# Kernel tuning notes

Hardware: AMD Instinct MI355X
Metric: run time of the kernel (lower is better)

The kernel has to match this reference:

```python
import jax, jax.numpy as jnp
import numpy as np

KSIZE = 7
FEAT_SIZE = 64
BETA = 0.02


def _resize_bilinear_ac(x, out_h, out_w):
    """Bilinear resize with align_corners=True. x: (B, C, H, W)."""
    H, W = x.shape[-2], x.shape[-1]
    ys = jnp.linspace(0.0, H - 1.0, out_h)
    xs = jnp.linspace(0.0, W - 1.0, out_w)
    y0 = jnp.clip(jnp.floor(ys).astype(jnp.int32), 0, H - 1)
    x0 = jnp.clip(jnp.floor(xs).astype(jnp.int32), 0, W - 1)
    y1 = jnp.minimum(y0 + 1, H - 1)
    x1 = jnp.minimum(x0 + 1, W - 1)
    wy = (ys - y0.astype(x.dtype))[None, None, :, None]
    wx = (xs - x0.astype(x.dtype))[None, None, None, :]
    rows = x[:, :, y0, :] * (1.0 - wy) + x[:, :, y1, :] * wy      # (B,C,out_h,W)
    out = rows[:, :, :, x0] * (1.0 - wx) + rows[:, :, :, x1] * wx  # (B,C,out_h,out_w)
    return out


def _sce(feat, w, b):
    """EfficientSpatialContextNet: shifted local-correlation context + 1x1 conv + relu."""
    B, C, h, wd = feat.shape
    k, pad = KSIZE, KSIZE // 2
    # F.normalize(p=2, dim=1) with eps=1e-12 (clamped norm)
    fn = feat / jnp.maximum(jnp.sqrt(jnp.sum(feat * feat, axis=1, keepdims=True)), 1e-12)
    fp = jnp.pad(fn, ((0, 0), (0, 0), (pad, pad), (pad, pad)))
    offsets = ([(i, i) for i in range(k)]
               + [(i, pad) for i in range(k)]
               + [(i, k - 1 - i) for i in range(k)]
               + [(pad, i) for i in range(k)])
    ctx = jnp.stack([jnp.sum(fp[:, :, r:h + r, c:wd + c] * fn, axis=1)
                     for (r, c) in offsets], axis=1)  # (B, 4k, h, w)
    out = jnp.concatenate([feat, ctx], axis=1)        # (B, C+4k, h, w)
    out = jnp.einsum('oc,bchw->bohw', w, out) + b[None, :, None, None]
    return jax.nn.relu(out)


def _l2norm(f):
    # FeatureL2Norm: eps added inside sqrt
    return f / jnp.sqrt(jnp.sum(f * f, axis=1, keepdims=True) + 1e-6)


def _forward(src_feat, tgt_feat, sce_w, sce_b):
    fs = FEAT_SIZE
    s = _l2norm(_sce(src_feat, sce_w, sce_b))
    t = _l2norm(_sce(tgt_feat, sce_w, sce_b))
    B, C, hs, ws = s.shape
    ht, wt = t.shape[2], t.shape[3]
    Ls, Lt = hs * ws, ht * wt
    corr = jnp.einsum('bcs,bct->bst', s.reshape(B, C, Ls), t.reshape(B, C, Lt))
    # mutual NN filter (Rocco et al.)
    smax = jnp.max(corr, axis=2, keepdims=True)
    tmax = jnp.max(corr, axis=1, keepdims=True)
    smax = jnp.where(smax == 0, 1e-30, smax)
    tmax = jnp.where(tmax == 0, 1e-30, tmax)
    corr = corr * ((corr / smax) * (corr / tmax))
    # resize corr on source grid, then on target grid (bilinear, align_corners=True)
    c_s2t = jnp.transpose(corr, (0, 2, 1)).reshape(B, Lt, hs, ws)
    c_s2t = _resize_bilinear_ac(c_s2t, fs, fs)                       # (B, Lt, fs, fs)
    c_t2s = jnp.transpose(c_s2t.reshape(B, Lt, fs * fs), (0, 2, 1)).reshape(B, fs * fs, ht, wt)
    c = _resize_bilinear_ac(c_t2s, fs, fs)                           # (B, fs*fs, fs, fs)
    # soft argmax with temperature (softmax over source positions)
    p = jax.nn.softmax(c / BETA, axis=1).reshape(B, fs, fs, fs, fs)  # (B, hs', ws', ht', wt')
    xn = jnp.linspace(-1.0, 1.0, fs).astype(c.dtype)
    yn = jnp.linspace(-1.0, 1.0, fs).astype(c.dtype)
    grid_x = jnp.einsum('bijhw,j->bhw', p, xn)
    grid_y = jnp.einsum('bijhw,i->bhw', p, yn)
    flow_norm = jnp.stack([grid_x, grid_y], axis=1)                  # (B, 2, fs, fs)
    # unnormalise mapping and convert to flow
    H = W = fs
    mx = (flow_norm[:, 0] + 1.0) * (W - 1) / 2.0
    my = (flow_norm[:, 1] + 1.0) * (H - 1) / 2.0
    xx = jnp.arange(W, dtype=flow_norm.dtype)[None, None, :]
    yy = jnp.arange(H, dtype=flow_norm.dtype)[None, :, None]
    flow = jnp.stack([mx - xx, my - yy], axis=1)                     # (B, 2, fs, fs)
    return flow


def setup_inputs() -> dict:
    key = jax.random.key(0)
    k1, k2, k3 = jax.random.split(key, 3)
    B, C, h, w = 4, 1024, 32, 32
    src_feat = jax.random.normal(k1, (B, C, h, w), dtype=jnp.float32)
    tgt_feat = jax.random.normal(k2, (B, C, h, w), dtype=jnp.float32)
    sce_w = jax.random.normal(k3, (2048, C + 4 * KSIZE), dtype=jnp.float32) * 0.03
    sce_b = jnp.zeros((2048,), dtype=jnp.float32)
    return {"src_feat": src_feat, "tgt_feat": tgt_feat, "sce_w": sce_w, "sce_b": sce_b}


def reference(src_feat, tgt_feat, sce_w, sce_b):
    return _forward(src_feat, tgt_feat, sce_w, sce_b)
```

## Files before the change

### kernel.cpp

```cpp
#include <hip/hip_runtime.h>
#include <math.h>

#define HW    1024
#define CIN   1024
#define CCTX  28
#define CALL  1052
#define COUT  2048
#define CCHNK 512

typedef _Float16 half8   __attribute__((ext_vector_type(8)));
typedef _Float16 half4_t __attribute__((ext_vector_type(4)));
typedef _Float16 half2_t __attribute__((ext_vector_type(2)));
typedef __fp16   fp16x2  __attribute__((ext_vector_type(2)));
typedef float    f32x4   __attribute__((ext_vector_type(4)));

__device__ __forceinline__ void split2(float a0, float a1, half2_t& h, half2_t& l) {
    float h0 = __uint_as_float(__float_as_uint(a0) & 0xFFFFE000u);
    float h1 = __uint_as_float(__float_as_uint(a1) & 0xFFFFE000u);
    fp16x2 hp = __builtin_amdgcn_cvt_pkrtz(h0, h1);
    fp16x2 lp = __builtin_amdgcn_cvt_pkrtz(a0 - h0, a1 - h1);
    h = __builtin_bit_cast(half2_t, hp);
    l = __builtin_bit_cast(half2_t, lp);
}
__device__ __forceinline__ void split4(float4 v, half4_t& h, half4_t& l) {
    half2_t ha, la, hb, lb;
    split2(v.x, v.y, ha, la);
    split2(v.z, v.w, hb, lb);
    h = __builtin_shufflevector(ha, hb, 0, 1, 2, 3);
    l = __builtin_shufflevector(la, lb, 0, 1, 2, 3);
}
__device__ __forceinline__ float f4get(const float4& v, int e) {
    return e == 0 ? v.x : e == 1 ? v.y : e == 2 ? v.z : v.w;
}

__global__ void pnorm_part(const float* __restrict__ src, const float* __restrict__ tgt,
                           float* __restrict__ parts) {
    int img = blockIdx.x, pb = blockIdx.y, part = blockIdx.z;
    int p = pb * 64 + threadIdx.x;
    const float* feat = ((img < 4) ? src + (size_t)img * CIN * HW
                                   : tgt + (size_t)(img - 4) * CIN * HW)
                        + (size_t)part * 256 * HW + p;
    float a4[4] = {};
    for (int c = 0; c < 256; c += 8) {
        float v[8];
#pragma unroll
        for (int j = 0; j < 8; ++j) v[j] = feat[(size_t)(c + j) * HW];
#pragma unroll
        for (int j = 0; j < 8; ++j) a4[j & 3] = fmaf(v[j], v[j], a4[j & 3]);
    }
    parts[(size_t)part * 8192 + img * 1024 + p] = (a4[0] + a4[1]) + (a4[2] + a4[3]);
}
__global__ void pnorm_combine(const float* __restrict__ parts, float* __restrict__ pnorm) {
    int img = blockIdx.x;
    int p = blockIdx.y * 64 + threadIdx.x;
    float s = parts[img * 1024 + p] + parts[8192 + img * 1024 + p]
            + parts[16384 + img * 1024 + p] + parts[24576 + img * 1024 + p];
    pnorm[img * HW + p] = fmaxf(sqrtf(s), 1e-12f);
}

__global__ void ctx_kernel(const float* __restrict__ src, const float* __restrict__ tgt,
                           const float* __restrict__ pnorm, float* __restrict__ ctx) {
    int img = blockIdx.x;
    int y = blockIdx.y;
    int tid = threadIdx.x;
    int o = tid >> 5;
    int x = tid & 31;
    const float* feat = (img < 4) ? src + (size_t)img * CIN * HW
                                  : tgt + (size_t)(img - 4) * CIN * HW;
    int g = o / 7, i = o % 7;
    int r, c;
    if (g == 0)      { r = i; c = i; }
    else if (g == 1) { r = i; c = 3; }
    else if (g == 2) { r = i; c = 6 - i; }
    else             { r = 3; c = i; }
    int y2 = y + r - 3, x2 = x + c - 3;
    int p = y * 32 + x;
    float outv = 0.f;
    if (y2 >= 0 && y2 < 32 && x2 >= 0 && x2 < 32) {
        int p2 = y2 * 32 + x2;
        const float* f0 = feat + p;
        const float* f1 = feat + p2;
        float a4[4] = {};
        for (int ch = 0; ch < CIN; ch += 8) {
            float va[8], vb[8];
#pragma unroll
            for (int j = 0; j < 8; ++j) {
                va[j] = f0[(size_t)(ch + j) * HW];
                vb[j] = f1[(size_t)(ch + j) * HW];
            }
#pragma unroll
            for (int j = 0; j < 8; ++j) a4[j & 3] = fmaf(va[j], vb[j], a4[j & 3]);
        }
        float acc = (a4[0] + a4[1]) + (a4[2] + a4[3]);
        outv = acc / (pnorm[img * HW + p] * pnorm[img * HW + p2]);
    }
    ctx[((size_t)img * CCTX + o) * HW + p] = outv;
}

#define ABUF_H 2560
#define BBUF_H 5120
#define BUF_H  15360
template <bool FIRST>
__global__ __launch_bounds__(256, 2) void conv_mfma(
    const float* __restrict__ src, const float* __restrict__ tgt,
    const float* __restrict__ ctxb, const float* __restrict__ w,
    const float* __restrict__ bias, float* __restrict__ ychunk,
    float* __restrict__ nrm_parts, int c0) {
    __shared__ __align__(16) _Float16 lds[2 * BUF_H];

    int cb = blockIdx.x, pb = blockIdx.y, img = blockIdx.z;
    int n0 = pb * 64, m0g = c0 + cb * 128;
    const float* feat = (img < 4) ? src + (size_t)img * CIN * HW
                                  : tgt + (size_t)(img - 4) * CIN * HW;
    const float* ctxi = ctxb + (size_t)img * CCTX * HW;
    int tid = threadIdx.x;
    int aq = tid & 15, ar = tid >> 4;
    int brow = tid >> 1, bh_ = tid & 1;

    float4 xa[2], xb[4];
    auto loadA = [&](int k0) {
#pragma unroll
        for (int j = 0; j < 2; ++j) {
            int k = k0 + ar * 2 + j;
            if (k < CIN)       xa[j] = *(const float4*)(feat + (size_t)k * HW + n0 + aq * 4);
            else if (k < CALL) xa[j] = *(const float4*)(ctxi + (size_t)(k - CIN) * HW + n0 + aq * 4);
            else               xa[j] = make_float4(0.f, 0.f, 0.f, 0.f);
        }
    };
    auto loadB = [&](int k0) {
#pragma unroll
        for (int i = 0; i < 4; ++i) {
            int k = k0 + bh_ * 16 + i * 4;
            xb[i] = (k < CALL) ? *(const float4*)(w + (size_t)(m0g + brow) * CALL + k)
                               : make_float4(0.f, 0.f, 0.f, 0.f);
        }
    };
    auto storeLDS = [&](int b) {
        _Float16* Ah = lds + b * BUF_H;
        _Float16* Al = Ah + ABUF_H;
        _Float16* Bh = Al + ABUF_H;
        _Float16* Bl = Bh + BBUF_H;
#pragma unroll
        for (int p = 0; p < 4; ++p) {
            half2_t h, l;
            split2(f4get(xa[0], p), f4get(xa[1], p), h, l);
            int row = aq * 4 + p;
            *(half2_t*)(Ah + row * 40 + ar * 2) = h;
            *(half2_t*)(Al + row * 40 + ar * 2) = l;
        }
#pragma unroll
        for (int i = 0; i < 4; ++i) {
            half4_t h, l;
            split4(xb[i], h, l);
            *(half4_t*)(Bh + brow * 40 + bh_ * 16 + i * 4) = h;
            *(half4_t*)(Bl + brow * 40 + bh_ * 16 + i * 4) = l;
        }
    };

    int lane = tid & 63, wv4 = tid >> 6;
    int wm = wv4 >> 1, wn = wv4 & 1;
    int frow = lane & 15, kcol = (lane >> 4) * 8;

    f32x4 acc[2][4] = {};
    const int NT = 33;
    loadA(0); loadB(0); storeLDS(0);
    __syncthreads();
    for (int t = 0; t < NT; ++t) {
        if (t + 1 < NT) { loadA((t + 1) * 32); loadB((t + 1) * 32); }
        const _Float16* Ah = lds + (t & 1) * BUF_H;
        const _Float16* Al = Ah + ABUF_H;
        const _Float16* Bh = Al + ABUF_H;
        const _Float16* Bl = Bh + BBUF_H;
        half8 ah[2], alr[2], bhr[4], blr[4];
#pragma unroll
        for (int fm = 0; fm < 2; ++fm) {
            int r = wm * 32 + fm * 16 + frow;
            ah[fm]  = *(const half8*)(Ah + r * 40 + kcol);
            alr[fm] = *(const half8*)(Al + r * 40 + kcol);
        }
#pragma unroll
        for (int fn = 0; fn < 4; ++fn) {
            int r = wn * 64 + fn * 16 + frow;
            bhr[fn] = *(const half8*)(Bh + r * 40 + kcol);
            blr[fn] = *(const half8*)(Bl + r * 40 + kcol);
        }
#pragma unroll
        for (int fm = 0; fm < 2; ++fm)
#pragma unroll
            for (int fn = 0; fn < 4; ++fn) {
                acc[fm][fn] = __builtin_amdgcn_mfma_f32_16x16x32_f16(ah[fm],  bhr[fn], acc[fm][fn], 0, 0, 0);
                acc[fm][fn] = __builtin_amdgcn_mfma_f32_16x16x32_f16(ah[fm],  blr[fn], acc[fm][fn], 0, 0, 0);
                acc[fm][fn] = __builtin_amdgcn_mfma_f32_16x16x32_f16(alr[fm], bhr[fn], acc[fm][fn], 0, 0, 0);
            }
        if (t + 1 < NT) storeLDS((t + 1) & 1);
        __syncthreads();
    }

    float* ybounce = (float*)lds;
    float* ns = ybounce + 64 * 132;
    float psum[2][4] = {};
#pragma unroll
    for (int fm = 0; fm < 2; ++fm)
#pragma unroll
        for (int fn = 0; fn < 4; ++fn) {
            int chan_l = wn * 64 + fn * 16 + (lane & 15);
            float bv = bias[m0g + chan_l];
#pragma unroll
            for (int r = 0; r < 4; ++r) {
                float v = fmaxf(acc[fm][fn][r] + bv, 0.f);
                int pix_l = wm * 32 + fm * 16 + (lane >> 4) * 4 + r;
                ybounce[pix_l * 132 + chan_l] = v;
                psum[fm][r] = fmaf(v, v, psum[fm][r]);
            }
        }
#pragma unroll
    for (int off = 1; off <= 8; off <<= 1)
#pragma unroll
        for (int fm = 0; fm < 2; ++fm)
#pragma unroll
            for (int r = 0; r < 4; ++r)
                psum[fm][r] = psum[fm][r] + __shfl_xor(psum[fm][r], off);
    if ((lane & 15) == 0) {
#pragma unroll
        for (int fm = 0; fm < 2; ++fm)
#pragma unroll
            for (int r = 0; r < 4; ++r)
                ns[wn * 64 + wm * 32 + fm * 16 + (lane >> 4) * 4 + r] = psum[fm][r];
    }
    __syncthreads();
    {
        int row = tid >> 2, seg = tid & 3;
        float* yp = ychunk + ((size_t)img * HW + n0 + row) * CCHNK + cb * 128 + seg * 32;
#pragma unroll
        for (int i = 0; i < 8; ++i)
            *(float4*)(yp + i * 4) = *(float4*)(ybounce + row * 132 + seg * 32 + i * 4);
    }
    if (tid < 64) {
        float sv = ns[tid] + ns[64 + tid];
        float* np = nrm_parts + ((size_t)img * 4 + cb) * HW + n0 + tid;
        if (FIRST) *np = sv; else *np += sv;
    }
}

template <int MODE>
__global__ __launch_bounds__(256, 2) void corr_mfma(
    const float* __restrict__ ychunk, const float* __restrict__ nrm_sq,
    float* __restrict__ corrT, float* __restrict__ spar, float* __restrict__ tpar) {
    __shared__ __align__(16) _Float16 lds[2 * BUF_H];

    int sb = blockIdx.x, tb = blockIdx.y, b = blockIdx.z;
    int t0 = tb * 64, s0 = sb * 128;
    const float* ytg = ychunk + (size_t)(4 + b) * HW * CCHNK;
    const float* ysr = ychunk + (size_t)b * HW * CCHNK;
    int tid = threadIdx.x;
    int arow = tid >> 2, akq = tid & 3;
    int brow = tid >> 1, bh_ = tid & 1;

    float4 xa[2], xb[4];
    auto loadAB = [&](int k0) {
#pragma unroll
        for (int i = 0; i < 2; ++i)
            xa[i] = *(const float4*)(ytg + (size_t)(t0 + arow) * CCHNK + k0 + akq * 8 + i * 4);
#pragma unroll
        for (int i = 0; i < 4; ++i)
            xb[i] = *(const float4*)(ysr + (size_t)(s0 + brow) * CCHNK + k0 + bh_ * 16 + i * 4);
    };
    auto storeLDS = [&](int bb) {
        _Float16* Ah = lds + bb * BUF_H;
        _Float16* Al = Ah + ABUF_H;
        _Float16* Bh = Al + ABUF_H;
        _Float16* Bl = Bh + BBUF_H;
#pragma unroll
        for (int i = 0; i < 2; ++i) {
            half4_t h, l;
            split4(xa[i], h, l);
            *(half4_t*)(Ah + arow * 40 + akq * 8 + i * 4) = h;
            *(half4_t*)(Al + arow * 40 + akq * 8 + i * 4) = l;
        }
#pragma unroll
        for (int i = 0; i < 4; ++i) {
            half4_t h, l;
            split4(xb[i], h, l);
            *(half4_t*)(Bh + brow * 40 + bh_ * 16 + i * 4) = h;
            *(half4_t*)(Bl + brow * 40 + bh_ * 16 + i * 4) = l;
        }
    };

    int lane = tid & 63, wv4 = tid >> 6;
    int wm = wv4 >> 1, wn = wv4 & 1;
    int frow = lane & 15, kcol = (lane >> 4) * 8;

    f32x4 acc[2][4] = {};
    const int NT = CCHNK / 32;
    loadAB(0); storeLDS(0);
    __syncthreads();
    for (int t = 0; t < NT; ++t) {
        if (t + 1 < NT) loadAB((t + 1) * 32);
        const _Float16* Ah = lds + (t & 1) * BUF_H;
        const _Float16* Al = Ah + ABUF_H;
        const _Float16* Bh = Al + ABUF_H;
        const _Float16* Bl = Bh + BBUF_H;
        half8 ah[2], alr[2], bhr[4], blr[4];
#pragma unroll
        for (int fm = 0; fm < 2; ++fm) {
            int r = wm * 32 + fm * 16 + frow;
            ah[fm]  = *(const half8*)(Ah + r * 40 + kcol);
            alr[fm] = *(const half8*)(Al + r * 40 + kcol);
        }
#pragma unroll
        for (int fn = 0; fn < 4; ++fn) {
            int r = wn * 64 + fn * 16 + frow;
            bhr[fn] = *(const half8*)(Bh + r * 40 + kcol);
            blr[fn] = *(const half8*)(Bl + r * 40 + kcol);
        }
#pragma unroll
        for (int fm = 0; fm < 2; ++fm)
#pragma unroll
            for (int fn = 0; fn < 4; ++fn) {
                acc[fm][fn] = __builtin_amdgcn_mfma_f32_16x16x32_f16(ah[fm],  bhr[fn], acc[fm][fn], 0, 0, 0);
                acc[fm][fn] = __builtin_amdgcn_mfma_f32_16x16x32_f16(ah[fm],  blr[fn], acc[fm][fn], 0, 0, 0);
                acc[fm][fn] = __builtin_amdgcn_mfma_f32_16x16x32_f16(alr[fm], bhr[fn], acc[fm][fn], 0, 0, 0);
            }
        if (t + 1 < NT) storeLDS((t + 1) & 1);
        __syncthreads();
    }

    float rnt[2][4], rns[4];
    float rowmax[2][4] = {};
    float colmax[4] = {};
    if (MODE == 2) {
#pragma unroll
        for (int fm = 0; fm < 2; ++fm)
#pragma unroll
            for (int r = 0; r < 4; ++r) {
                int t = t0 + wm * 32 + fm * 16 + (lane >> 4) * 4 + r;
                rnt[fm][r] = 1.f / sqrtf(nrm_sq[(size_t)(4 + b) * HW + t] + 1e-6f);
            }
#pragma unroll
        for (int fn = 0; fn < 4; ++fn) {
            int s_ = s0 + wn * 64 + fn * 16 + (lane & 15);
            rns[fn] = 1.f / sqrtf(nrm_sq[(size_t)b * HW + s_] + 1e-6f);
        }
    }
#pragma unroll
    for (int fm = 0; fm < 2; ++fm)
#pragma unroll
        for (int r = 0; r < 4; ++r) {
            int t = t0 + wm * 32 + fm * 16 + (lane >> 4) * 4 + r;
            float* cp = corrT + ((size_t)b * HW + t) * HW + s0 + wn * 64 + (lane & 15);
#pragma unroll
            for (int fn = 0; fn < 4; ++fn) {
                float v = acc[fm][fn][r];
                if (MODE >= 1) v += cp[fn * 16];
                if (MODE == 2) {
                    v *= rnt[fm][r] * rns[fn];
                    rowmax[fm][r] = fmaxf(rowmax[fm][r], v);
                    colmax[fn] = fmaxf(colmax[fn], v);
                }
                cp[fn * 16] = v;
            }
        }
    if (MODE == 2) {
        float* rm = (float*)lds;
        float* cm = rm + 128;
#pragma unroll
        for (int off = 1; off <= 8; off <<= 1)
#pragma unroll
            for (int fm = 0; fm < 2; ++fm)
#pragma unroll
                for (int r = 0; r < 4; ++r)
                    rowmax[fm][r] = fmaxf(rowmax[fm][r], __shfl_xor(rowmax[fm][r], off));
        if ((lane & 15) == 0) {
#pragma unroll
            for (int fm = 0; fm < 2; ++fm)
#pragma unroll
                for (int r = 0; r < 4; ++r)
                    rm[wn * 64 + wm * 32 + fm * 16 + (lane >> 4) * 4 + r] = rowmax[fm][r];
        }
#pragma unroll
        for (int off = 16; off <= 32; off <<= 1)
#pragma unroll
            for (int fn = 0; fn < 4; ++fn)
                colmax[fn] = fmaxf(colmax[fn], __shfl_xor(colmax[fn], off));
        if ((lane >> 4) == 0) {
#pragma unroll
            for (int fn = 0; fn < 4; ++fn)
                cm[wv4 * 64 + fn * 16 + (lane & 15)] = colmax[fn];
        }
        __syncthreads();
        if (tid < 64)
            tpar[((size_t)b * 8 + sb) * HW + t0 + tid] = fmaxf(rm[tid], rm[64 + tid]);
        if (tid < 128) {
            int q = tid >> 6;
            float mv = fmaxf(cm[q * 64 + (tid & 63)], cm[(2 + q) * 64 + (tid & 63)]);
            spar[((size_t)b * 16 + tb) * HW + s0 + tid] = mv;
        }
    }
}

__global__ void nrm_reduce(const float* __restrict__ nrm_parts, float* __restrict__ nrm_sq) {
    int img = blockIdx.y;
    int p = blockIdx.x * 256 + threadIdx.x;
    float s = 0.f;
#pragma unroll
    for (int mb = 0; mb < 4; ++mb)
        s += nrm_parts[((size_t)img * 4 + mb) * HW + p];
    nrm_sq[img * HW + p] = s;
}

__global__ void combine_max(const float* __restrict__ spar, const float* __restrict__ tpar,
                            float* __restrict__ smax, float* __restrict__ tmax) {
    int b = blockIdx.y;
    int i = blockIdx.x * 256 + threadIdx.x;
    float m = 0.f;
#pragma unroll
    for (int q = 0; q < 16; ++q) m = fmaxf(m, spar[((size_t)b * 16 + q) * HW + i]);
    smax[b * HW + i] = m;
    float m2 = 0.f;
#pragma unroll
    for (int q = 0; q < 8; ++q) m2 = fmaxf(m2, tpar[((size_t)b * 8 + q) * HW + i]);
    tmax[b * HW + i] = m2;
}

__global__ __launch_bounds__(256) void final_kernel(const float* __restrict__ corrT,
                                                    const float* __restrict__ smax,
                                                    const float* __restrict__ tmax,
                                                    float* __restrict__ out) {
    __shared__ float vsh[1024];
    __shared__ float rbuf[16];
    int b = blockIdx.z;
    int typ = blockIdx.y;
    int txp = blockIdx.x;
    int tid = threadIdx.x;

    float fy = typ * (31.0f / 63.0f);
    int y0 = min((int)fy, 31); int y1 = min(y0 + 1, 31);
    float wy = fy - (float)y0;
    float fx = txp * (31.0f / 63.0f);
    int x0 = min((int)fx, 31); int x1 = min(x0 + 1, 31);
    float wx = fx - (float)x0;
    int tA = y0 * 32 + x0, tB = y0 * 32 + x1, tC = y1 * 32 + x0, tD = y1 * 32 + x1;
    const float* base = corrT + (size_t)b * HW * HW;
    const float* rA = base + (size_t)tA * HW;
    const float* rB = base + (size_t)tB * HW;
    const float* rC = base + (size_t)tC * HW;
    const float* rD = base + (size_t)tD * HW;
    float tmA_ = tmax[b * HW + tA]; if (tmA_ == 0.f) tmA_ = 1e-30f;
    float tmB_ = tmax[b * HW + tB]; if (tmB_ == 0.f) tmB_ = 1e-30f;
    float tmC_ = tmax[b * HW + tC]; if (tmC_ == 0.f) tmC_ = 1e-30f;
    float tmD_ = tmax[b * HW + tD]; if (tmD_ == 0.f) tmD_ = 1e-30f;
    float itA = 1.f / tmA_, itB = 1.f / tmB_, itC = 1.f / tmC_, itD = 1.f / tmD_;
    float wA = (1.f - wy) * (1.f - wx), wB = (1.f - wy) * wx;
    float wC = wy * (1.f - wx), wD = wy * wx;
#pragma unroll
    for (int u = 0; u < 4; ++u) {
        int s = u * 256 + tid;
        float sm = smax[b * HW + s]; if (sm == 0.f) sm = 1e-30f;
        float is = 1.f / sm;
        float a = rA[s]; a = a * a * a * is * itA;
        float b2 = rB[s]; b2 = b2 * b2 * b2 * is * itB;
        float c2 = rC[s]; c2 = c2 * c2 * c2 * is * itC;
        float d2 = rD[s]; d2 = d2 * d2 * d2 * is * itD;
        vsh[s] = wA * a + wB * b2 + wC * c2 + wD * d2;
    }
    __syncthreads();

    int jx = tid & 63;
    int wvq = tid >> 6;
    float gxx = jx * (31.0f / 63.0f);
    int sx0 = min((int)gxx, 31), sx1 = min(sx0 + 1, 31);
    float wxx = gxx - (float)sx0, iwxx = 1.f - wxx;
    float xnj = jx * (2.0f / 63.0f) - 1.0f;

    float cv[16];
    float lmax = -1e30f;
#pragma unroll
    for (int u = 0; u < 16; ++u) {
        int iy = u * 4 + wvq;
        float gy = iy * (31.0f / 63.0f);
        int sy0 = min((int)gy, 31), sy1 = min(sy0 + 1, 31);
        float wyy = gy - (float)sy0;
        float r0 = vsh[sy0 * 32 + sx0] * iwxx + vsh[sy0 * 32 + sx1] * wxx;
        float r1 = vsh[sy1 * 32 + sx0] * iwxx + vsh[sy1 * 32 + sx1] * wxx;
        cv[u] = (r0 * (1.f - wyy) + r1 * wyy) * 50.0f;
        lmax = fmaxf(lmax, cv[u]);
    }
#pragma unroll
    for (int off = 32; off >= 1; off >>= 1) lmax = fmaxf(lmax, __shfl_down(lmax, off));
    int lane = tid & 63;
    if (lane == 0) rbuf[wvq] = lmax;
    __syncthreads();
    if (tid == 0) {
        float m = rbuf[0];
        for (int i = 1; i < 4; ++i) m = fmaxf(m, rbuf[i]);
        rbuf[0] = m;
    }
    __syncthreads();
    float m = rbuf[0];

    float e0 = 0.f, ex = 0.f, ey = 0.f;
#pragma unroll
    for (int u = 0; u < 16; ++u) {
        int iy = u * 4 + wvq;
        float e = __expf(cv[u] - m);
        e0 += e;
        ex = fmaf(e, xnj, ex);
        ey = fmaf(e, iy * (2.0f / 63.0f) - 1.0f, ey);
    }
#pragma unroll
    for (int off = 32; off >= 1; off >>= 1) {
        e0 += __shfl_down(e0, off);
        ex += __shfl_down(ex, off);
        ey += __shfl_down(ey, off);
    }
    if (lane == 0) { rbuf[4 + wvq] = e0; rbuf[8 + wvq] = ex; rbuf[12 + wvq] = ey; }
    __syncthreads();
    if (tid == 0) {
        float s0 = rbuf[4] + rbuf[5] + rbuf[6] + rbuf[7];
        float sx = rbuf[8] + rbuf[9] + rbuf[10] + rbuf[11];
        float sy = rbuf[12] + rbuf[13] + rbuf[14] + rbuf[15];
        float gx = sx / s0, gy = sy / s0;
        float mx = (gx + 1.f) * 31.5f;
        float my = (gy + 1.f) * 31.5f;
        out[(((size_t)b * 2 + 0) * 64 + typ) * 64 + txp] = mx - (float)txp;
        out[(((size_t)b * 2 + 1) * 64 + typ) * 64 + txp] = my - (float)typ;
    }
}

extern "C" void kernel_launch(void* const* d_in, const int* in_sizes, int n_in,
                              void* d_out, int out_size, void* d_ws, size_t ws_size,
                              hipStream_t stream) {
    const float* src  = (const float*)d_in[0];
    const float* tgt  = (const float*)d_in[1];
    const float* sw   = (const float*)d_in[2];
    const float* sb   = (const float*)d_in[3];
    float* out = (float*)d_out;

    float* corrT      = (float*)d_ws;
    float* nrm_parts  = corrT + 4194304;
    float* tpar       = nrm_parts + 32768;
    float* nrm_sq     = nrm_parts + 65536;
    float* smax       = nrm_sq + 8192;
    float* spar       = smax + 4096;
    float* tmax       = spar + 65536;
    float* pnorm      = tmax + 4096;
    float* ctxbuf     = pnorm + 8192;
    float* ychunk     = ctxbuf + 229376;
    float* pparts     = ychunk;

    pnorm_part<<<dim3(8, 16, 4), 64, 0, stream>>>(src, tgt, pparts);
    pnorm_combine<<<dim3(8, 16), 64, 0, stream>>>(pparts, pnorm);
    ctx_kernel<<<dim3(8, 32), 896, 0, stream>>>(src, tgt, pnorm, ctxbuf);

    conv_mfma<true><<<dim3(4, 16, 8), 256, 0, stream>>>(src, tgt, ctxbuf, sw, sb,
                                                        ychunk, nrm_parts, 0);
    corr_mfma<0><<<dim3(8, 16, 4), 256, 0, stream>>>(ychunk, nrm_sq, corrT, spar, tpar);
    for (int c = 1; c < 3; ++c) {
        conv_mfma<false><<<dim3(4, 16, 8), 256, 0, stream>>>(src, tgt, ctxbuf, sw, sb,
                                                             ychunk, nrm_parts, c * CCHNK);
        corr_mfma<1><<<dim3(8, 16, 4), 256, 0, stream>>>(ychunk, nrm_sq, corrT, spar, tpar);
    }
    conv_mfma<false><<<dim3(4, 16, 8), 256, 0, stream>>>(src, tgt, ctxbuf, sw, sb,
                                                         ychunk, nrm_parts, 3 * CCHNK);
    nrm_reduce<<<dim3(4, 8), 256, 0, stream>>>(nrm_parts, nrm_sq);
    corr_mfma<2><<<dim3(8, 16, 4), 256, 0, stream>>>(ychunk, nrm_sq, corrT, spar, tpar);

    combine_max<<<dim3(4, 4), 256, 0, stream>>>(spar, tpar, smax, tmax);
    final_kernel<<<dim3(64, 64, 4), 256, 0, stream>>>(corrT, smax, tmax, out);
}
```

Before: 531.3 us.

## Store conv output as pre-split fp16 hi/lo and read it directly in corr GEMM

The conv kernel now writes its intermediate as two fp16 hi/lo arrays instead of fp32, so the correlation GEMM can load MFMA fragments straight from global memory with no LDS staging or per-tile split. Conv tiles grow to 64x256 output per block with a single LDS buffer, and corr tiles grow to 128x128 per block, which halves the grid sizes and the partial-max buffers. The ctx dot-product loop is simplified to a plain serial FMA chain. The changes aim at less split work and better reuse per block, but they cost more registers, give fewer blocks in flight, and make the corr kernel read global memory without reuse through shared memory.

```diff
diff --git a/kernel.cpp b/kernel.cpp
--- a/kernel.cpp
+++ b/kernel.cpp
@@ -80,45 +80,39 @@
         int p2 = y2 * 32 + x2;
         const float* f0 = feat + p;
         const float* f1 = feat + p2;
-        float a4[4] = {};
-        for (int ch = 0; ch < CIN; ch += 8) {
-            float va[8], vb[8];
-#pragma unroll
-            for (int j = 0; j < 8; ++j) {
-                va[j] = f0[(size_t)(ch + j) * HW];
-                vb[j] = f1[(size_t)(ch + j) * HW];
-            }
-#pragma unroll
-            for (int j = 0; j < 8; ++j) a4[j & 3] = fmaf(va[j], vb[j], a4[j & 3]);
-        }
-        float acc = (a4[0] + a4[1]) + (a4[2] + a4[3]);
+        float acc = 0.f;
+        for (int ch = 0; ch < CIN; ++ch)
+            acc = fmaf(f0[(size_t)ch * HW], f1[(size_t)ch * HW], acc);
         outv = acc / (pnorm[img * HW + p] * pnorm[img * HW + p2]);
     }
     ctx[((size_t)img * CCTX + o) * HW + p] = outv;
 }
 
-#define ABUF_H 2560
-#define BBUF_H 5120
-#define BUF_H  15360
 template <bool FIRST>
-__global__ __launch_bounds__(256, 2) void conv_mfma(
+__global__ __launch_bounds__(256) void conv_mfma(
     const float* __restrict__ src, const float* __restrict__ tgt,
     const float* __restrict__ ctxb, const float* __restrict__ w,
-    const float* __restrict__ bias, float* __restrict__ ychunk,
-    float* __restrict__ nrm_parts, int c0) {
-    __shared__ __align__(16) _Float16 lds[2 * BUF_H];
+    const float* __restrict__ bias, _Float16* __restrict__ yh,
+    _Float16* __restrict__ yl, float* __restrict__ nrm_parts, int c0) {
+    __shared__ __align__(16) char smem[51200];
+    _Float16* Ah = (_Float16*)smem;
+    _Float16* Al = Ah + 2560;
+    _Float16* Wh = Al + 2560;
+    _Float16* Wl = Wh + 10240;
 
     int cb = blockIdx.x, pb = blockIdx.y, img = blockIdx.z;
-    int n0 = pb * 64, m0g = c0 + cb * 128;
+    int n0 = pb * 64;
+    int m0g = c0 + cb * 256;
     const float* feat = (img < 4) ? src + (size_t)img * CIN * HW
                                   : tgt + (size_t)(img - 4) * CIN * HW;
     const float* ctxi = ctxb + (size_t)img * CCTX * HW;
     int tid = threadIdx.x;
+    int lane = tid & 63, wv = tid >> 6;
+    int frow = lane & 15, kg = (lane >> 4) * 8;
     int aq = tid & 15, ar = tid >> 4;
-    int brow = tid >> 1, bh_ = tid & 1;
-
-    float4 xa[2], xb[4];
-    auto loadA = [&](int k0) {
+
+    float4 xa[2], xw[8];
+    auto stage_regs = [&](int k0) {
 #pragma unroll
         for (int j = 0; j < 2; ++j) {
             int k = k0 + ar * 2 + j;
@@ -126,20 +120,14 @@
             else if (k < CALL) xa[j] = *(const float4*)(ctxi + (size_t)(k - CIN) * HW + n0 + aq * 4);
             else               xa[j] = make_float4(0.f, 0.f, 0.f, 0.f);
         }
+#pragma unroll
+        for (int i = 0; i < 8; ++i) {
+            int k = k0 + i * 4;
+            xw[i] = (k + 4 <= CALL) ? *(const float4*)(w + (size_t)(m0g + tid) * CALL + k)
+                                    : make_float4(0.f, 0.f, 0.f, 0.f);
+        }
     };
-    auto loadB = [&](int k0) {
-#pragma unroll
-        for (int i = 0; i < 4; ++i) {
-            int k = k0 + bh_ * 16 + i * 4;
-            xb[i] = (k < CALL) ? *(const float4*)(w + (size_t)(m0g + brow) * CALL + k)
-                               : make_float4(0.f, 0.f, 0.f, 0.f);
-        }
-    };
-    auto storeLDS = [&](int b) {
-        _Float16* Ah = lds + b * BUF_H;
-        _Float16* Al = Ah + ABUF_H;
-        _Float16* Bh = Al + ABUF_H;
-        _Float16* Bl = Bh + BBUF_H;
+    auto write_lds = [&]() {
 #pragma unroll
         for (int p = 0; p < 4; ++p) {
             half2_t h, l;
@@ -149,205 +137,193 @@
             *(half2_t*)(Al + row * 40 + ar * 2) = l;
         }
 #pragma unroll
-        for (int i = 0; i < 4; ++i) {
+        for (int i = 0; i < 8; ++i) {
             half4_t h, l;
-            split4(xb[i], h, l);
-            *(half4_t*)(Bh + brow * 40 + bh_ * 16 + i * 4) = h;
-            *(half4_t*)(Bl + brow * 40 + bh_ * 16 + i * 4) = l;
+            split4(xw[i], h, l);
+            *(half4_t*)(Wh + tid * 40 + i * 4) = h;
+            *(half4_t*)(Wl + tid * 40 + i * 4) = l;
         }
     };
 
-    int lane = tid & 63, wv4 = tid >> 6;
-    int wm = wv4 >> 1, wn = wv4 & 1;
-    int frow = lane & 15, kcol = (lane >> 4) * 8;
-
-    f32x4 acc[2][4] = {};
+    f32x4 acc[4][4] = {};
     const int NT = 33;
-    loadA(0); loadB(0); storeLDS(0);
+    stage_regs(0); write_lds();
     __syncthreads();
     for (int t = 0; t < NT; ++t) {
-        if (t + 1 < NT) { loadA((t + 1) * 32); loadB((t + 1) * 32); }
-        const _Float16* Ah = lds + (t & 1) * BUF_H;
-        const _Float16* Al = Ah + ABUF_H;
-        const _Float16* Bh = Al + ABUF_H;
-        const _Float16* Bl = Bh + BBUF_H;
-        half8 ah[2], alr[2], bhr[4], blr[4];
-#pragma unroll
-        for (int fm = 0; fm < 2; ++fm) {
-            int r = wm * 32 + fm * 16 + frow;
-            ah[fm]  = *(const half8*)(Ah + r * 40 + kcol);
-            alr[fm] = *(const half8*)(Al + r * 40 + kcol);
+        half8 afh[4], afl[4], bfh[4], bfl[4];
+#pragma unroll
+        for (int fm = 0; fm < 4; ++fm) {
+            int r = fm * 16 + frow;
+            afh[fm] = *(const half8*)(Ah + r * 40 + kg);
+            afl[fm] = *(const half8*)(Al + r * 40 + kg);
         }
 #pragma unroll
         for (int fn = 0; fn < 4; ++fn) {
-            int r = wn * 64 + fn * 16 + frow;
-            bhr[fn] = *(const half8*)(Bh + r * 40 + kcol);
-            blr[fn] = *(const half8*)(Bl + r * 40 + kcol);
-        }
-#pragma unroll
-        for (int fm = 0; fm < 2; ++fm)
+            int r = wv * 64 + fn * 16 + frow;
+            bfh[fn] = *(const half8*)(Wh + r * 40 + kg);
+            bfl[fn] = *(const half8*)(Wl + r * 40 + kg);
+        }
+        if (t + 1 < NT) stage_regs((t + 1) * 32);
+#pragma unroll
+        for (int fm = 0; fm < 4; ++fm)
 #pragma unroll
             for (int fn = 0; fn < 4; ++fn) {
-                acc[fm][fn] = __builtin_amdgcn_mfma_f32_16x16x32_f16(ah[fm],  bhr[fn], acc[fm][fn], 0, 0, 0);
-                acc[fm][fn] = __builtin_amdgcn_mfma_f32_16x16x32_f16(ah[fm],  blr[fn], acc[fm][fn], 0, 0, 0);
-                acc[fm][fn] = __builtin_amdgcn_mfma_f32_16x16x32_f16(alr[fm], bhr[fn], acc[fm][fn], 0, 0, 0);
-            }
-        if (t + 1 < NT) storeLDS((t + 1) & 1);
+                acc[fm][fn] = __builtin_amdgcn_mfma_f32_16x16x32_f16(afh[fm], bfh[fn], acc[fm][fn], 0, 0, 0);
+                acc[fm][fn] = __builtin_amdgcn_mfma_f32_16x16x32_f16(afh[fm], bfl[fn], acc[fm][fn], 0, 0, 0);
+                acc[fm][fn] = __builtin_amdgcn_mfma_f32_16x16x32_f16(afl[fm], bfh[fn], acc[fm][fn], 0, 0, 0);
+            }
         __syncthreads();
-    }
-
-    float* ybounce = (float*)lds;
-    float* ns = ybounce + 64 * 132;
-    float psum[2][4] = {};
-#pragma unroll
-    for (int fm = 0; fm < 2; ++fm)
-#pragma unroll
-        for (int fn = 0; fn < 4; ++fn) {
-            int chan_l = wn * 64 + fn * 16 + (lane & 15);
-            float bv = bias[m0g + chan_l];
+        if (t + 1 < NT) write_lds();
+        __syncthreads();
+    }
+
+    float bv[4];
+#pragma unroll
+    for (int fn = 0; fn < 4; ++fn) bv[fn] = bias[m0g + wv * 64 + fn * 16 + frow];
+
+    float* nsf = (float*)smem;
+    _Float16* yb = (_Float16*)(smem + 2048);
+    float psum[4][4] = {};
+#pragma unroll
+    for (int fm = 0; fm < 4; ++fm)
+#pragma unroll
+        for (int fn = 0; fn < 4; ++fn)
 #pragma unroll
             for (int r = 0; r < 4; ++r) {
-                float v = fmaxf(acc[fm][fn][r] + bv, 0.f);
-                int pix_l = wm * 32 + fm * 16 + (lane >> 4) * 4 + r;
-                ybounce[pix_l * 132 + chan_l] = v;
+                float v = fmaxf(acc[fm][fn][r] + bv[fn], 0.f);
+                acc[fm][fn][r] = v;
                 psum[fm][r] = fmaf(v, v, psum[fm][r]);
             }
-        }
 #pragma unroll
     for (int off = 1; off <= 8; off <<= 1)
 #pragma unroll
-        for (int fm = 0; fm < 2; ++fm)
+        for (int fm = 0; fm < 4; ++fm)
 #pragma unroll
             for (int r = 0; r < 4; ++r)
                 psum[fm][r] = psum[fm][r] + __shfl_xor(psum[fm][r], off);
-    if ((lane & 15) == 0) {
-#pragma unroll
-        for (int fm = 0; fm < 2; ++fm)
+    if (frow == 0) {
+#pragma unroll
+        for (int fm = 0; fm < 4; ++fm)
 #pragma unroll
             for (int r = 0; r < 4; ++r)
-                ns[wn * 64 + wm * 32 + fm * 16 + (lane >> 4) * 4 + r] = psum[fm][r];
-    }
+                nsf[wv * 64 + fm * 16 + (lane >> 4) * 4 + r] = psum[fm][r];
+    }
+    __syncthreads();
+    float sv = 0.f;
+    if (tid < 64)
+        sv = nsf[tid] + nsf[64 + tid] + nsf[128 + tid] + nsf[192 + tid];
+#pragma unroll
+    for (int fm = 0; fm < 4; ++fm)
+#pragma unroll
+        for (int fn = 0; fn < 4; ++fn)
+#pragma unroll
+            for (int r = 0; r < 4; ++r) {
+                float v = acc[fm][fn][r];
+                float hf = __uint_as_float(__float_as_uint(v) & 0xFFFFE000u);
+                int pix_l = fm * 16 + (lane >> 4) * 4 + r;
+                int chan_l = wv * 64 + fn * 16 + frow;
+                yb[pix_l * 264 + chan_l] = (_Float16)hf;
+            }
     __syncthreads();
     {
         int row = tid >> 2, seg = tid & 3;
-        float* yp = ychunk + ((size_t)img * HW + n0 + row) * CCHNK + cb * 128 + seg * 32;
+        _Float16* gp = yh + ((size_t)img * HW + n0 + row) * CCHNK + cb * 256 + seg * 64;
 #pragma unroll
         for (int i = 0; i < 8; ++i)
-            *(float4*)(yp + i * 4) = *(float4*)(ybounce + row * 132 + seg * 32 + i * 4);
+            *(half8*)(gp + i * 8) = *(const half8*)(yb + row * 264 + seg * 64 + i * 8);
+    }
+    __syncthreads();
+#pragma unroll
+    for (int fm = 0; fm < 4; ++fm)
+#pragma unroll
+        for (int fn = 0; fn < 4; ++fn)
+#pragma unroll
+            for (int r = 0; r < 4; ++r) {
+                float v = acc[fm][fn][r];
+                float hf = __uint_as_float(__float_as_uint(v) & 0xFFFFE000u);
+                int pix_l = fm * 16 + (lane >> 4) * 4 + r;
+                int chan_l = wv * 64 + fn * 16 + frow;
+                yb[pix_l * 264 + chan_l] = (_Float16)(v - hf);
+            }
+    __syncthreads();
+    {
+        int row = tid >> 2, seg = tid & 3;
+        _Float16* gp = yl + ((size_t)img * HW + n0 + row) * CCHNK + cb * 256 + seg * 64;
+#pragma unroll
+        for (int i = 0; i < 8; ++i)
+            *(half8*)(gp + i * 8) = *(const half8*)(yb + row * 264 + seg * 64 + i * 8);
     }
     if (tid < 64) {
-        float sv = ns[tid] + ns[64 + tid];
-        float* np = nrm_parts + ((size_t)img * 4 + cb) * HW + n0 + tid;
+        float* np = nrm_parts + ((size_t)img * 2 + cb) * HW + n0 + tid;
         if (FIRST) *np = sv; else *np += sv;
     }
 }
 
 template <int MODE>
-__global__ __launch_bounds__(256, 2) void corr_mfma(
-    const float* __restrict__ ychunk, const float* __restrict__ nrm_sq,
-    float* __restrict__ corrT, float* __restrict__ spar, float* __restrict__ tpar) {
-    __shared__ __align__(16) _Float16 lds[2 * BUF_H];
-
+__global__ __launch_bounds__(256) void corr_mfma(
+    const _Float16* __restrict__ yh, const _Float16* __restrict__ yl,
+    const float* __restrict__ nrm_sq, float* __restrict__ corrT,
+    float* __restrict__ spar, float* __restrict__ tpar) {
+    __shared__ float rm[2][128];
+    __shared__ float cm[2][128];
     int sb = blockIdx.x, tb = blockIdx.y, b = blockIdx.z;
-    int t0 = tb * 64, s0 = sb * 128;
-    const float* ytg = ychunk + (size_t)(4 + b) * HW * CCHNK;
-    const float* ysr = ychunk + (size_t)b * HW * CCHNK;
-    int tid = threadIdx.x;
-    int arow = tid >> 2, akq = tid & 3;
-    int brow = tid >> 1, bh_ = tid & 1;
-
-    float4 xa[2], xb[4];
-    auto loadAB = [&](int k0) {
-#pragma unroll
-        for (int i = 0; i < 2; ++i)
-            xa[i] = *(const float4*)(ytg + (size_t)(t0 + arow) * CCHNK + k0 + akq * 8 + i * 4);
-#pragma unroll
-        for (int i = 0; i < 4; ++i)
-            xb[i] = *(const float4*)(ysr + (size_t)(s0 + brow) * CCHNK + k0 + bh_ * 16 + i * 4);
-    };
-    auto storeLDS = [&](int bb) {
-        _Float16* Ah = lds + bb * BUF_H;
-        _Float16* Al = Ah + ABUF_H;
-        _Float16* Bh = Al + ABUF_H;
-        _Float16* Bl = Bh + BBUF_H;
-#pragma unroll
-        for (int i = 0; i < 2; ++i) {
-            half4_t h, l;
-            split4(xa[i], h, l);
-            *(half4_t*)(Ah + arow * 40 + akq * 8 + i * 4) = h;
-            *(half4_t*)(Al + arow * 40 + akq * 8 + i * 4) = l;
-        }
-#pragma unroll
-        for (int i = 0; i < 4; ++i) {
-            half4_t h, l;
-            split4(xb[i], h, l);
-            *(half4_t*)(Bh + brow * 40 + bh_ * 16 + i * 4) = h;
-            *(half4_t*)(Bl + brow * 40 + bh_ * 16 + i * 4) = l;
-        }
-    };
-
-    int lane = tid & 63, wv4 = tid >> 6;
-    int wm = wv4 >> 1, wn = wv4 & 1;
-    int frow = lane & 15, kcol = (lane >> 4) * 8;
-
-    f32x4 acc[2][4] = {};
-    const int NT = CCHNK / 32;
-    loadAB(0); storeLDS(0);
-    __syncthreads();
-    for (int t = 0; t < NT; ++t) {
-        if (t + 1 < NT) loadAB((t + 1) * 32);
-        const _Float16* Ah = lds + (t & 1) * BUF_H;
-        const _Float16* Al = Ah + ABUF_H;
-        const _Float16* Bh = Al + ABUF_H;
-        const _Float16* Bl = Bh + BBUF_H;
-        half8 ah[2], alr[2], bhr[4], blr[4];
-#pragma unroll
-        for (int fm = 0; fm < 2; ++fm) {
-            int r = wm * 32 + fm * 16 + frow;
-            ah[fm]  = *(const half8*)(Ah + r * 40 + kcol);
-            alr[fm] = *(const half8*)(Al + r * 40 + kcol);
-        }
-#pragma unroll
-        for (int fn = 0; fn < 4; ++fn) {
-            int r = wn * 64 + fn * 16 + frow;
-            bhr[fn] = *(const half8*)(Bh + r * 40 + kcol);
-            blr[fn] = *(const half8*)(Bl + r * 40 + kcol);
-        }
-#pragma unroll
-        for (int fm = 0; fm < 2; ++fm)
+    int tid = threadIdx.x, lane = tid & 63, wv = tid >> 6;
+    int wm = wv >> 1, wn = wv & 1;
+    int frow = lane & 15, kg = (lane >> 4) * 8;
+
+    size_t trow = (size_t)(4 + b) * HW + tb * 128 + wm * 64 + frow;
+    size_t srow = (size_t)b * HW + sb * 128 + wn * 64 + frow;
+    const _Float16* ahp = yh + trow * CCHNK + kg;
+    const _Float16* alp = yl + trow * CCHNK + kg;
+    const _Float16* bhp = yh + srow * CCHNK + kg;
+    const _Float16* blp = yl + srow * CCHNK + kg;
+
+    f32x4 acc[4][4] = {};
+#pragma unroll 2
+    for (int t = 0; t < 16; ++t) {
+        int k0 = t * 32;
+        half8 ah[4], al_[4], bh[4], bl[4];
+#pragma unroll
+        for (int f = 0; f < 4; ++f) {
+            size_t ro = (size_t)f * 16 * CCHNK + k0;
+            ah[f]  = *(const half8*)(ahp + ro);
+            al_[f] = *(const half8*)(alp + ro);
+            bh[f]  = *(const half8*)(bhp + ro);
+            bl[f]  = *(const half8*)(blp + ro);
+        }
+#pragma unroll
+        for (int fm = 0; fm < 4; ++fm)
 #pragma unroll
             for (int fn = 0; fn < 4; ++fn) {
-                acc[fm][fn] = __builtin_amdgcn_mfma_f32_16x16x32_f16(ah[fm],  bhr[fn], acc[fm][fn], 0, 0, 0);
-                acc[fm][fn] = __builtin_amdgcn_mfma_f32_16x16x32_f16(ah[fm],  blr[fn], acc[fm][fn], 0, 0, 0);
-                acc[fm][fn] = __builtin_amdgcn_mfma_f32_16x16x32_f16(alr[fm], bhr[fn], acc[fm][fn], 0, 0, 0);
-            }
-        if (t + 1 < NT) storeLDS((t + 1) & 1);
-        __syncthreads();
-    }
-
-    float rnt[2][4], rns[4];
-    float rowmax[2][4] = {};
+                acc[fm][fn] = __builtin_amdgcn_mfma_f32_16x16x32_f16(ah[fm],  bh[fn], acc[fm][fn], 0, 0, 0);
+                acc[fm][fn] = __builtin_amdgcn_mfma_f32_16x16x32_f16(ah[fm],  bl[fn], acc[fm][fn], 0, 0, 0);
+                acc[fm][fn] = __builtin_amdgcn_mfma_f32_16x16x32_f16(al_[fm], bh[fn], acc[fm][fn], 0, 0, 0);
+            }
+    }
+
+    float rnt[4][4], rns[4];
+    float rowmax[4][4] = {};
     float colmax[4] = {};
     if (MODE == 2) {
 #pragma unroll
-        for (int fm = 0; fm < 2; ++fm)
+        for (int fm = 0; fm < 4; ++fm)
 #pragma unroll
             for (int r = 0; r < 4; ++r) {
-                int t = t0 + wm * 32 + fm * 16 + (lane >> 4) * 4 + r;
+                int t = tb * 128 + wm * 64 + fm * 16 + (lane >> 4) * 4 + r;
                 rnt[fm][r] = 1.f / sqrtf(nrm_sq[(size_t)(4 + b) * HW + t] + 1e-6f);
             }
 #pragma unroll
         for (int fn = 0; fn < 4; ++fn) {
-            int s_ = s0 + wn * 64 + fn * 16 + (lane & 15);
+            int s_ = sb * 128 + wn * 64 + fn * 16 + frow;
             rns[fn] = 1.f / sqrtf(nrm_sq[(size_t)b * HW + s_] + 1e-6f);
         }
     }
 #pragma unroll
-    for (int fm = 0; fm < 2; ++fm)
+    for (int fm = 0; fm < 4; ++fm)
 #pragma unroll
         for (int r = 0; r < 4; ++r) {
-            int t = t0 + wm * 32 + fm * 16 + (lane >> 4) * 4 + r;
-            float* cp = corrT + ((size_t)b * HW + t) * HW + s0 + wn * 64 + (lane & 15);
+            int t = tb * 128 + wm * 64 + fm * 16 + (lane >> 4) * 4 + r;
+            float* cp = corrT + ((size_t)b * HW + t) * HW + sb * 128 + wn * 64 + frow;
 #pragma unroll
             for (int fn = 0; fn < 4; ++fn) {
                 float v = acc[fm][fn][r];
@@ -361,51 +337,43 @@
             }
         }
     if (MODE == 2) {
-        float* rm = (float*)lds;
-        float* cm = rm + 128;
 #pragma unroll
         for (int off = 1; off <= 8; off <<= 1)
 #pragma unroll
-            for (int fm = 0; fm < 2; ++fm)
+            for (int fm = 0; fm < 4; ++fm)
 #pragma unroll
                 for (int r = 0; r < 4; ++r)
                     rowmax[fm][r] = fmaxf(rowmax[fm][r], __shfl_xor(rowmax[fm][r], off));
-        if ((lane & 15) == 0) {
-#pragma unroll
-            for (int fm = 0; fm < 2; ++fm)
+        if (frow == 0) {
+#pragma unroll
+            for (int fm = 0; fm < 4; ++fm)
 #pragma unroll
                 for (int r = 0; r < 4; ++r)
-                    rm[wn * 64 + wm * 32 + fm * 16 + (lane >> 4) * 4 + r] = rowmax[fm][r];
+                    rm[wn][wm * 64 + fm * 16 + (lane >> 4) * 4 + r] = rowmax[fm][r];
         }
 #pragma unroll
         for (int off = 16; off <= 32; off <<= 1)
 #pragma unroll
             for (int fn = 0; fn < 4; ++fn)
                 colmax[fn] = fmaxf(colmax[fn], __shfl_xor(colmax[fn], off));
-        if ((lane >> 4) == 0) {
+        if (lane < 16) {
 #pragma unroll
             for (int fn = 0; fn < 4; ++fn)
-                cm[wv4 * 64 + fn * 16 + (lane & 15)] = colmax[fn];
+                cm[wm][wn * 64 + fn * 16 + lane] = colmax[fn];
         }
         __syncthreads();
-        if (tid < 64)
-            tpar[((size_t)b * 8 + sb) * HW + t0 + tid] = fmaxf(rm[tid], rm[64 + tid]);
-        if (tid < 128) {
-            int q = tid >> 6;
-            float mv = fmaxf(cm[q * 64 + (tid & 63)], cm[(2 + q) * 64 + (tid & 63)]);
-            spar[((size_t)b * 16 + tb) * HW + s0 + tid] = mv;
-        }
+        if (tid < 128)
+            tpar[((size_t)b * 8 + sb) * HW + tb * 128 + tid] = fmaxf(rm[0][tid], rm[1][tid]);
+        if (tid < 128)
+            spar[((size_t)b * 8 + tb) * HW + sb * 128 + tid] = fmaxf(cm[0][tid], cm[1][tid]);
     }
 }
 
 __global__ void nrm_reduce(const float* __restrict__ nrm_parts, float* __restrict__ nrm_sq) {
     int img = blockIdx.y;
     int p = blockIdx.x * 256 + threadIdx.x;
-    float s = 0.f;
-#pragma unroll
-    for (int mb = 0; mb < 4; ++mb)
-        s += nrm_parts[((size_t)img * 4 + mb) * HW + p];
-    nrm_sq[img * HW + p] = s;
+    nrm_sq[img * HW + p] = nrm_parts[((size_t)img * 2 + 0) * HW + p]
+                         + nrm_parts[((size_t)img * 2 + 1) * HW + p];
 }
 
 __global__ void combine_max(const float* __restrict__ spar, const float* __restrict__ tpar,
@@ -414,7 +382,7 @@
     int i = blockIdx.x * 256 + threadIdx.x;
     float m = 0.f;
 #pragma unroll
-    for (int q = 0; q < 16; ++q) m = fmaxf(m, spar[((size_t)b * 16 + q) * HW + i]);
+    for (int q = 0; q < 8; ++q) m = fmaxf(m, spar[((size_t)b * 8 + q) * HW + i]);
     smax[b * HW + i] = m;
     float m2 = 0.f;
 #pragma unroll
@@ -536,34 +504,36 @@
     const float* sb   = (const float*)d_in[3];
     float* out = (float*)d_out;
 
-    float* corrT      = (float*)d_ws;
-    float* nrm_parts  = corrT + 4194304;
-    float* tpar       = nrm_parts + 32768;
-    float* nrm_sq     = nrm_parts + 65536;
-    float* smax       = nrm_sq + 8192;
-    float* spar       = smax + 4096;
-    float* tmax       = spar + 65536;
-    float* pnorm      = tmax + 4096;
-    float* ctxbuf     = pnorm + 8192;
-    float* ychunk     = ctxbuf + 229376;
-    float* pparts     = ychunk;
+    float* f = (float*)d_ws;
+    float*     corrT     = f;
+    _Float16*  yh        = (_Float16*)(f + 4194304);
+    _Float16*  yl        = (_Float16*)(f + 4194304 + 2097152);
+    float*     nrm_parts = f + 8388608;
+    float*     tpar      = nrm_parts + 16384;
+    float*     nrm_sq    = tpar + 32768;
+    float*     smax      = nrm_sq + 8192;
+    float*     spar      = smax + 4096;
+    float*     tmax      = spar + 32768;
+    float*     pnorm     = tmax + 4096;
+    float*     ctxbuf    = pnorm + 8192;
+    float*     pparts    = (float*)yh;
 
     pnorm_part<<<dim3(8, 16, 4), 64, 0, stream>>>(src, tgt, pparts);
     pnorm_combine<<<dim3(8, 16), 64, 0, stream>>>(pparts, pnorm);
     ctx_kernel<<<dim3(8, 32), 896, 0, stream>>>(src, tgt, pnorm, ctxbuf);
 
-    conv_mfma<true><<<dim3(4, 16, 8), 256, 0, stream>>>(src, tgt, ctxbuf, sw, sb,
-                                                        ychunk, nrm_parts, 0);
-    corr_mfma<0><<<dim3(8, 16, 4), 256, 0, stream>>>(ychunk, nrm_sq, corrT, spar, tpar);
+    conv_mfma<true><<<dim3(2, 16, 8), 256, 0, stream>>>(src, tgt, ctxbuf, sw, sb,
+                                                        yh, yl, nrm_parts, 0);
+    corr_mfma<0><<<dim3(8, 8, 4), 256, 0, stream>>>(yh, yl, nrm_sq, corrT, spar, tpar);
     for (int c = 1; c < 3; ++c) {
-        conv_mfma<false><<<dim3(4, 16, 8), 256, 0, stream>>>(src, tgt, ctxbuf, sw, sb,
-                                                             ychunk, nrm_parts, c * CCHNK);
-        corr_mfma<1><<<dim3(8, 16, 4), 256, 0, stream>>>(ychunk, nrm_sq, corrT, spar, tpar);
-    }
-    conv_mfma<false><<<dim3(4, 16, 8), 256, 0, stream>>>(src, tgt, ctxbuf, sw, sb,
-                                                         ychunk, nrm_parts, 3 * CCHNK);
+        conv_mfma<false><<<dim3(2, 16, 8), 256, 0, stream>>>(src, tgt, ctxbuf, sw, sb,
+                                                             yh, yl, nrm_parts, c * CCHNK);
+        corr_mfma<1><<<dim3(8, 8, 4), 256, 0, stream>>>(yh, yl, nrm_sq, corrT, spar, tpar);
+    }
+    conv_mfma<false><<<dim3(2, 16, 8), 256, 0, stream>>>(src, tgt, ctxbuf, sw, sb,
+                                                         yh, yl, nrm_parts, 3 * CCHNK);
     nrm_reduce<<<dim3(4, 8), 256, 0, stream>>>(nrm_parts, nrm_sq);
-    corr_mfma<2><<<dim3(8, 16, 4), 256, 0, stream>>>(ychunk, nrm_sq, corrT, spar, tpar);
+    corr_mfma<2><<<dim3(8, 8, 4), 256, 0, stream>>>(yh, yl, nrm_sq, corrT, spar, tpar);
 
     combine_max<<<dim3(4, 4), 256, 0, stream>>>(spar, tpar, smax, tmax);
     final_kernel<<<dim3(64, 64, 4), 256, 0, stream>>>(corrT, smax, tmax, out);
```

After: 633.5 us. 1.19x slower.
